# Kernel tuning notes

Hardware: AMD Instinct MI355X
Metric: run time of the kernel (lower is better)

Reference implementation:

```python
import jax, jax.numpy as jnp
import numpy as np

T, H, I, E, K, G, TG = 8192, 2048, 1024, 64, 8, 8, 4
ROUTED_SCALE = 2.5


def setup_inputs() -> dict:
    key = jax.random.key(0)
    ks = jax.random.split(key, 7)
    s = 0.02  # weight init scale
    return {
        "hidden_states": jax.random.normal(ks[0], (T, H), jnp.float32),
        "gate_w": jax.random.normal(ks[1], (E, H), jnp.float32) * s,
        "e_bias": jax.random.normal(ks[2], (E,), jnp.float32) * s,
        "w_gate_up": jax.random.normal(ks[3], (E, H, 2 * I), jnp.float32) * s,
        "w_down": jax.random.normal(ks[4], (E, I, H), jnp.float32) * s,
        "shared_gate_up": jax.random.normal(ks[5], (H, 2 * I), jnp.float32) * s,
        "shared_down": jax.random.normal(ks[6], (I, H), jnp.float32) * s,
    }


def silu_and_mul(x):
    g, u = jnp.split(x, 2, axis=-1)
    return jax.nn.silu(g) * u


def grouped_topk(router_logits, e_bias):
    # sigmoid scoring with e_score_correction_bias (DeepSeek-V3 / GLM4-MoE style)
    scores = jax.nn.sigmoid(router_logits)            # [T, E]
    scores_for_choice = scores + e_bias[None, :]
    # group score = sum of top-2 biased scores in each group
    grp = scores_for_choice.reshape(-1, G, E // G)
    group_scores = jax.lax.top_k(grp, 2)[0].sum(-1)   # [T, G]
    _, gidx = jax.lax.top_k(group_scores, TG)         # [T, TG]
    tok = jnp.arange(scores.shape[0])[:, None]
    group_mask = jnp.zeros_like(group_scores, dtype=bool).at[tok, gidx].set(True)
    expert_mask = jnp.repeat(group_mask, E // G, axis=-1)  # [T, E]
    masked = jnp.where(expert_mask, scores_for_choice, -jnp.inf)
    _, topk_ids = jax.lax.top_k(masked, K)            # [T, K]
    # combine weights come from the *unbiased* sigmoid scores
    topk_w = jnp.take_along_axis(scores, topk_ids, axis=-1)
    topk_w = topk_w / jnp.sum(topk_w, axis=-1, keepdims=True)  # renormalize
    return topk_w, topk_ids


def reference(hidden_states, gate_w, e_bias, w_gate_up, w_down,
              shared_gate_up, shared_down):
    x = hidden_states                                  # [T, H]
    # gate runs in fp32
    router_logits = x.astype(jnp.float32) @ gate_w.T   # [T, E]
    topk_w, topk_ids = grouped_topk(router_logits, e_bias)

    # shared expert MLP
    shared_out = silu_and_mul(x @ shared_gate_up) @ shared_down  # [T, H]

    # dense [T, E] combine matrix (top-k sparse in values)
    tok = jnp.arange(x.shape[0])[:, None]
    route = jnp.zeros((x.shape[0], E), x.dtype).at[tok, topk_ids].set(
        topk_w.astype(x.dtype))

    # grouped expert GEMMs via scan over experts (bounds peak memory)
    def body(acc, params):
        w1, w2, rw = params                            # [H,2I], [I,H], [T]
        y = silu_and_mul(x @ w1) @ w2                  # [T, H]
        return acc + rw[:, None] * y, None

    acc0 = jnp.zeros_like(x)
    routed_out, _ = jax.lax.scan(body, acc0, (w_gate_up, w_down, route.T))

    return routed_out * ROUTED_SCALE + shared_out
```

## Files before the change

kernel.cpp:

```cpp
#include <hip/hip_runtime.h>
#include <stdint.h>

#define T_TOK 8192
#define HDIM  2048
#define IDIM  1024
#define NEXP  64
#define KTOP  8
#define TGRP  4
#define TKTOT (T_TOK*KTOP)
#define MAXITEMS 4096
#define RSCALE 2.5f

typedef __attribute__((ext_vector_type(8))) short short8;
typedef __attribute__((ext_vector_type(4))) float f32x4;

__device__ __forceinline__ float bf2f(uint16_t u) {
    union { unsigned i; float f; } v; v.i = ((unsigned)u) << 16; return v.f;
}
__device__ __forceinline__ uint16_t f2bf(float f) {
    union { float f; unsigned i; } v; v.f = f;
    unsigned r = (v.i + 0x7FFFu + ((v.i >> 16) & 1u)) >> 16;
    return (uint16_t)r;
}
__device__ __forceinline__ void gload_lds16(const void* g, void* l) {
    __builtin_amdgcn_global_load_lds(
        (const __attribute__((address_space(1))) void*)g,
        (__attribute__((address_space(3))) void*)l, 16, 0, 0);
}
__device__ __forceinline__ int imin(int a, int b) { return a < b ? a : b; }

__global__ __launch_bounds__(256) void k_router(
    const float* __restrict__ x, const float* __restrict__ gw,
    const float* __restrict__ ebias,
    int* __restrict__ topk_ids, float* __restrict__ topk_w,
    int* __restrict__ counts)
{
    __shared__ float xs[16][132];
    __shared__ float wsb[64][133];
    __shared__ float sc[16][65];
    __shared__ float su[16][65];
    const int tid = threadIdx.x;
    const int e = tid & 63;
    const int tg = tid >> 6;
    const long tblk = (long)blockIdx.x * 16;

    float acc0 = 0.f, acc1 = 0.f, acc2 = 0.f, acc3 = 0.f;
    for (int ch = 0; ch < 16; ++ch) {
        const int h0 = ch << 7;
        for (int i = tid; i < 512; i += 256) {
            int r = i >> 5, c4 = (i & 31) << 2;
            float4 v = *(const float4*)(x + (tblk + r) * HDIM + h0 + c4);
            *(float4*)&xs[r][c4] = v;
        }
        for (int i = tid; i < 8192; i += 256) {
            int r = i >> 7, c = i & 127;
            wsb[r][c] = gw[(long)r * HDIM + h0 + c];
        }
        __syncthreads();
        #pragma unroll 8
        for (int hh = 0; hh < 128; ++hh) {
            float wv = wsb[e][hh];
            acc0 += xs[tg][hh] * wv;
            acc1 += xs[tg + 4][hh] * wv;
            acc2 += xs[tg + 8][hh] * wv;
            acc3 += xs[tg + 12][hh] * wv;
        }
        __syncthreads();
    }
    const float be = ebias[e];
    {
        float s;
        s = 1.f / (1.f + expf(-acc0)); su[tg][e] = s;      sc[tg][e] = s + be;
        s = 1.f / (1.f + expf(-acc1)); su[tg + 4][e] = s;  sc[tg + 4][e] = s + be;
        s = 1.f / (1.f + expf(-acc2)); su[tg + 8][e] = s;  sc[tg + 8][e] = s + be;
        s = 1.f / (1.f + expf(-acc3)); su[tg + 12][e] = s; sc[tg + 12][e] = s + be;
    }
    __syncthreads();
    if (tid < 16) {
        const int t = tid;
        float gs[8];
        #pragma unroll
        for (int g = 0; g < 8; ++g) {
            float m1 = -1e30f, m2 = -1e30f;
            #pragma unroll
            for (int j = 0; j < 8; ++j) {
                float v = sc[t][g * 8 + j];
                if (v > m1) { m2 = m1; m1 = v; } else if (v > m2) { m2 = v; }
            }
            gs[g] = m1 + m2;
        }
        int selmask = 0;
        #pragma unroll
        for (int it = 0; it < TGRP; ++it) {
            float best = -1e30f; int bg = 0;
            #pragma unroll
            for (int g = 0; g < 8; ++g)
                if (!((selmask >> g) & 1) && gs[g] > best) { best = gs[g]; bg = g; }
            selmask |= (1 << bg);
        }
        unsigned long long chosen = 0ull;
        int ids[KTOP]; float wv[KTOP]; float wsum = 0.f;
        #pragma unroll
        for (int it = 0; it < KTOP; ++it) {
            float best = -1e30f; int bi = 0;
            for (int ee = 0; ee < 64; ++ee) {
                if (((selmask >> (ee >> 3)) & 1) && !((chosen >> ee) & 1ull)) {
                    float v = sc[t][ee];
                    if (v > best) { best = v; bi = ee; }
                }
            }
            chosen |= (1ull << bi);
            ids[it] = bi; wv[it] = su[t][bi]; wsum += wv[it];
        }
        const float inv = 1.f / wsum;
        #pragma unroll
        for (int k = 0; k < KTOP; ++k) {
            topk_ids[(tblk + t) * KTOP + k] = ids[k];
            topk_w[(tblk + t) * KTOP + k] = wv[k] * inv;
            atomicAdd(&counts[ids[k]], 1);
        }
    }
}

__global__ __launch_bounds__(64) void k_scan2(
    const int* __restrict__ counts, int* offsets, int* cursor,
    int* __restrict__ it_r0, int* __restrict__ it_end,
    int* __restrict__ it_e, int* __restrict__ it_n0, int* __restrict__ nitems)
{
    const int e = threadIdx.x;
    const int c = counts[e];
    int pre = c;
    #pragma unroll
    for (int d = 1; d < 64; d <<= 1) {
        int v = __shfl_up(pre, d, 64);
        if (e >= d) pre += v;
    }
    const int offE = pre - c;
    offsets[e] = offE; cursor[e] = offE;
    const int ntl = (c + 255) >> 8;
    int ipre = ntl;
    #pragma unroll
    for (int d = 1; d < 64; d <<= 1) {
        int v = __shfl_up(ipre, d, 64);
        if (e >= d) ipre += v;
    }
    const int ibase = (ipre - ntl) * 8;
    for (int p = 0; p < 8; ++p)
        for (int t = 0; t < ntl; ++t) {
            int idx = ibase + p * ntl + t;
            it_r0[idx] = offE + t * 256;
            it_end[idx] = offE + c;
            it_e[idx] = e;
            it_n0[idx] = p << 8;
        }
    if (e == 63) *nitems = ibase + ntl * 8;
}

__global__ __launch_bounds__(256) void k_scatter(
    const int* __restrict__ topk_ids, int* cursor,
    int* __restrict__ perm_token, int* __restrict__ slot_of)
{
    int i = blockIdx.x * 256 + threadIdx.x;
    if (i >= TKTOT) return;
    int e = topk_ids[i];
    int pos = atomicAdd(&cursor[e], 1);
    perm_token[pos] = i >> 3;
    slot_of[i] = pos;
}

__global__ __launch_bounds__(256) void k_cvt_bf16(
    const float* __restrict__ in, uint16_t* __restrict__ outp, long n4)
{
    long i = (long)blockIdx.x * 256 + threadIdx.x;
    if (i >= n4) return;
    float4 v = *(const float4*)(in + i * 4);
    uint64_t pk = (uint64_t)f2bf(v.x) | ((uint64_t)f2bf(v.y) << 16)
                | ((uint64_t)f2bf(v.z) << 32) | ((uint64_t)f2bf(v.w) << 48);
    *(uint64_t*)(outp + i * 4) = pk;
}

template<bool INTER>
__global__ __launch_bounds__(256) void k_transpose2(
    const float* __restrict__ src, uint16_t* __restrict__ dst,
    int R, int C, long sStride, long dStride)
{
    __shared__ float tile[64][65];
    const int c0 = blockIdx.x << 6, r0 = blockIdx.y << 6, s = blockIdx.z;
    const float* S = src + (long)s * sStride;
    uint16_t* D = dst + (long)s * dStride;
    const int lc = (threadIdx.x & 15) << 2;
    const int lr = threadIdx.x >> 4;
    #pragma unroll
    for (int p = 0; p < 4; ++p) {
        int y = lr + p * 16;
        float4 v = *(const float4*)(S + (long)(r0 + y) * C + c0 + lc);
        tile[y][lc] = v.x; tile[y][lc + 1] = v.y;
        tile[y][lc + 2] = v.z; tile[y][lc + 3] = v.w;
    }
    __syncthreads();
    const int wc = threadIdx.x >> 3;
    const int wx = (threadIdx.x & 7) << 3;
    #pragma unroll
    for (int p = 0; p < 2; ++p) {
        int c = wc + p * 32;
        short8 v;
        #pragma unroll
        for (int j = 0; j < 8; ++j) v[j] = (short)f2bf(tile[wx + j][c]);
        int cg = c0 + c;
        int rd = INTER ? (((cg & (IDIM - 1)) << 1) + (cg >> 10)) : cg;
        *(short8*)(D + (long)rd * R + r0 + wx) = v;
    }
}

template<bool GATEUP, bool ROUTED>
__global__ __launch_bounds__(512, 2) void k_gemm3(
    const uint16_t* __restrict__ A, const uint16_t* __restrict__ Bw,
    void* __restrict__ OutP,
    const int* __restrict__ perm_token,
    const int* __restrict__ it_r0, const int* __restrict__ it_end,
    const int* __restrict__ it_e, const int* __restrict__ it_n0,
    const int* __restrict__ nitems, int* __restrict__ qcur,
    int Kd, long expStride)
{
    __shared__ char ldsb[4 * 32768];
    __shared__ int s_item;
    const int tid = threadIdx.x, lane = tid & 63, wid = tid >> 6;
    const int wm = wid >> 2, wn = wid & 3;

    const int rchunk = lane >> 2;
    const int swzS = ((lane & 3) ^ ((lane >> 3) & 3)) << 3;
    const int swzR = ((lane >> 4) ^ ((lane >> 1) & 3)) << 4;
    const int aoff = (wm * 128 + (lane & 15)) * 64 + swzR;
    const int boff = (wn * 64 + (lane & 15)) * 64 + swzR;
    const int ldst0 = (wid * 2) * 1024;
    const int ldst1 = (wid * 2 + 1) * 1024;

    const int nSub = Kd >> 5;
    const int NI = ROUTED ? nitems[0] : 0;

    for (;;) {
        int row0, end, n0; long eoff;
        if (ROUTED) {
            __syncthreads();
            if (tid == 0) s_item = atomicAdd(qcur, 1);
            __syncthreads();
            const int it = s_item;
            if (it >= NI) break;
            row0 = it_r0[it]; end = it_end[it]; n0 = it_n0[it];
            eoff = (long)it_e[it] * expStride;
        } else {
            row0 = (int)(blockIdx.x >> 3) << 8;
            end = row0 + 256;
            n0 = (int)(blockIdx.x & 7) << 8;
            eoff = 0;
        }

        const uint16_t *pA0, *pA1, *pB0, *pB1;
        {
            int r0l = (wid * 2) * 16 + rchunk;
            int r1l = (wid * 2 + 1) * 16 + rchunk;
            int ra0 = row0 + r0l, ra1 = row0 + r1l;
            if (ROUTED) { ra0 = imin(ra0, end - 1); ra1 = imin(ra1, end - 1); }
            long ga0 = (GATEUP && ROUTED) ? (long)perm_token[ra0] : (long)ra0;
            long ga1 = (GATEUP && ROUTED) ? (long)perm_token[ra1] : (long)ra1;
            pA0 = A + ga0 * Kd + swzS;
            pA1 = A + ga1 * Kd + swzS;
            pB0 = Bw + eoff + (long)(n0 + r0l) * Kd + swzS;
            pB1 = Bw + eoff + (long)(n0 + r1l) * Kd + swzS;
        }

        f32x4 acc[8][4];
        #pragma unroll
        for (int f = 0; f < 8; ++f)
            #pragma unroll
            for (int g = 0; g < 4; ++g) { f32x4 z = {0.f,0.f,0.f,0.f}; acc[f][g] = z; }

        #pragma unroll
        for (int j = 0; j < 3; ++j) {
            char* bb = ldsb + j * 32768;
            gload_lds16(pA0 + (j << 5), bb + ldst0);
            gload_lds16(pA1 + (j << 5), bb + ldst1);
            gload_lds16(pB0 + (j << 5), bb + 16384 + ldst0);
            gload_lds16(pB1 + (j << 5), bb + 16384 + ldst1);
        }

        for (int j = 0; j < nSub; ++j) {
            asm volatile("s_waitcnt vmcnt(8)" ::: "memory");
            __builtin_amdgcn_s_barrier();
            if (j + 3 < nSub) {
                const int js = j + 3;
                char* bb = ldsb + (js & 3) * 32768;
                gload_lds16(pA0 + (js << 5), bb + ldst0);
                gload_lds16(pA1 + (js << 5), bb + ldst1);
                gload_lds16(pB0 + (js << 5), bb + 16384 + ldst0);
                gload_lds16(pB1 + (js << 5), bb + 16384 + ldst1);
            }
            const char* bb = ldsb + (j & 3) * 32768;
            short8 av[8], bv[4];
            #pragma unroll
            for (int f = 0; f < 8; ++f)
                av[f] = *(const short8*)(bb + aoff + f * 1024);
            #pragma unroll
            for (int g = 0; g < 4; ++g)
                bv[g] = *(const short8*)(bb + 16384 + boff + g * 1024);
            __builtin_amdgcn_s_setprio(1);
            #pragma unroll
            for (int f = 0; f < 8; ++f)
                #pragma unroll
                for (int g = 0; g < 4; ++g)
                    acc[f][g] = __builtin_amdgcn_mfma_f32_16x16x32_bf16(
                        av[f], bv[g], acc[f][g], 0, 0, 0);
            __builtin_amdgcn_s_setprio(0);
        }

        const int colb = n0 + wn * 64 + (lane & 15);
        const int rowbase = row0 + wm * 128 + ((lane >> 4) << 2);
        if (GATEUP) {
            uint16_t* Oact = (uint16_t*)OutP;
            const bool evenl = ((lane & 1) == 0);
            #pragma unroll
            for (int f = 0; f < 8; ++f)
                #pragma unroll
                for (int g = 0; g < 4; ++g) {
                    f32x4 v = acc[f][g];
                    #pragma unroll
                    for (int r = 0; r < 4; ++r) {
                        float gg = v[r];
                        float uu = __shfl_xor(gg, 1, 64);
                        int row = rowbase + f * 16 + r;
                        if (evenl && (!ROUTED || row < end)) {
                            int jcol = (colb + g * 16) >> 1;
                            float sg = gg / (1.f + __expf(-gg));
                            Oact[(long)row * IDIM + jcol] = f2bf(sg * uu);
                        }
                    }
                }
        } else if (ROUTED) {
            uint16_t* Y = (uint16_t*)OutP;
            #pragma unroll
            for (int f = 0; f < 8; ++f)
                #pragma unroll
                for (int g = 0; g < 4; ++g) {
                    f32x4 v = acc[f][g];
                    #pragma unroll
                    for (int r = 0; r < 4; ++r) {
                        int row = rowbase + f * 16 + r;
                        if (row < end)
                            Y[(long)row * HDIM + colb + g * 16] = f2bf(v[r]);
                    }
                }
        } else {
            float* O = (float*)OutP;
            #pragma unroll
            for (int f = 0; f < 8; ++f)
                #pragma unroll
                for (int g = 0; g < 4; ++g) {
                    f32x4 v = acc[f][g];
                    #pragma unroll
                    for (int r = 0; r < 4; ++r) {
                        int row = rowbase + f * 16 + r;
                        O[(long)row * HDIM + colb + g * 16] = v[r];
                    }
                }
        }
        if (!ROUTED) break;
    }
}

__global__ __launch_bounds__(256) void k_combine(
    float* __restrict__ out, const uint16_t* __restrict__ ybuf,
    const int* __restrict__ slot_of, const float* __restrict__ topk_w)
{
    __shared__ int sl[KTOP];
    __shared__ float sw[KTOP];
    const int t = blockIdx.x, tid = threadIdx.x;
    if (tid < KTOP) {
        sl[tid] = slot_of[t * KTOP + tid];
        sw[tid] = topk_w[t * KTOP + tid] * RSCALE;
    }
    __syncthreads();
    const int h0 = tid << 3;
    float* orow = out + (long)t * HDIM + h0;
    float4 v0 = *(const float4*)(orow);
    float4 v1 = *(const float4*)(orow + 4);
    float a[8] = { v0.x, v0.y, v0.z, v0.w, v1.x, v1.y, v1.z, v1.w };
    #pragma unroll
    for (int k = 0; k < KTOP; ++k) {
        const uint16_t* yr = ybuf + (long)sl[k] * HDIM + h0;
        short8 y = *(const short8*)yr;
        float w = sw[k];
        #pragma unroll
        for (int j = 0; j < 8; ++j)
            a[j] += w * bf2f((uint16_t)y[j]);
    }
    v0.x = a[0]; v0.y = a[1]; v0.z = a[2]; v0.w = a[3];
    v1.x = a[4]; v1.y = a[5]; v1.z = a[6]; v1.w = a[7];
    *(float4*)(orow) = v0;
    *(float4*)(orow + 4) = v1;
}

extern "C" void kernel_launch(void* const* d_in, const int* in_sizes, int n_in,
                              void* d_out, int out_size, void* d_ws, size_t ws_size,
                              hipStream_t stream)
{
    const float* x  = (const float*)d_in[0];
    const float* gw = (const float*)d_in[1];
    const float* eb = (const float*)d_in[2];
    const float* w1 = (const float*)d_in[3];
    const float* w2 = (const float*)d_in[4];
    const float* s1 = (const float*)d_in[5];
    const float* s2 = (const float*)d_in[6];
    float* out = (float*)d_out;
    char* ws = (char*)d_ws;

    size_t off = 0;
    auto take = [&](size_t b) { size_t r = off; off += (b + 255) & ~(size_t)255; return r; };
    const size_t oXBF = take((size_t)T_TOK * HDIM * 2);
    const size_t oACT = take((size_t)TKTOT * IDIM * 2);
    const size_t oASH = take((size_t)T_TOK * IDIM * 2);
    const size_t oW1T = take((size_t)NEXP * 2048 * 2048 * 2);
    const size_t oW2T = take((size_t)NEXP * 2048 * 1024 * 2);
    const size_t oS1T = take((size_t)2048 * 2048 * 2);
    const size_t oS2T = take((size_t)2048 * 1024 * 2);
    const size_t oTKI = take((size_t)TKTOT * 4);
    const size_t oTKW = take((size_t)TKTOT * 4);
    const size_t oSLT = take((size_t)TKTOT * 4);
    const size_t oPRM = take((size_t)TKTOT * 4);
    const size_t oCTL = take(1024);
    const size_t oOFS = take(256);
    const size_t oCUR = take(256);
    const size_t oNT  = take(256);
    const size_t oIR  = take(MAXITEMS * 4);
    const size_t oIE  = take(MAXITEMS * 4);
    const size_t oIX  = take(MAXITEMS * 4);
    const size_t oIN  = take(MAXITEMS * 4);
    (void)ws_size; (void)in_sizes; (void)n_in; (void)out_size;

    uint16_t* xbf  = (uint16_t*)(ws + oXBF);
    uint16_t* act  = (uint16_t*)(ws + oACT);
    uint16_t* ash  = (uint16_t*)(ws + oASH);
    uint16_t* w1t  = (uint16_t*)(ws + oW1T);
    uint16_t* ybuf = (uint16_t*)(ws + oW1T);
    uint16_t* w2t  = (uint16_t*)(ws + oW2T);
    uint16_t* s1t  = (uint16_t*)(ws + oS1T);
    uint16_t* s2t  = (uint16_t*)(ws + oS2T);
    int*   tki  = (int*)(ws + oTKI);
    float* tkw  = (float*)(ws + oTKW);
    int*   slot = (int*)(ws + oSLT);
    int*   prm  = (int*)(ws + oPRM);
    int*   ctl  = (int*)(ws + oCTL);
    int*   ofs  = (int*)(ws + oOFS);
    int*   cur  = (int*)(ws + oCUR);
    int*   nt   = (int*)(ws + oNT);
    int*   ir0  = (int*)(ws + oIR);
    int*   iend = (int*)(ws + oIE);
    int*   ie   = (int*)(ws + oIX);
    int*   in0  = (int*)(ws + oIN);

    hipMemsetAsync(ws + oCTL, 0, 1024, stream);

    k_router<<<T_TOK / 16, 256, 0, stream>>>(x, gw, eb, tki, tkw, ctl);
    k_scan2<<<1, 64, 0, stream>>>(ctl, ofs, cur, ir0, iend, ie, in0, nt);
    k_scatter<<<TKTOT / 256, 256, 0, stream>>>(tki, cur, prm, slot);

    k_cvt_bf16<<<(T_TOK * HDIM / 4 + 255) / 256, 256, 0, stream>>>(x, xbf, (long)T_TOK * HDIM / 4);
    k_transpose2<true ><<<dim3(32, 32, NEXP), 256, 0, stream>>>(w1, w1t, 2048, 2048,
        (long)2048 * 2048, (long)2048 * 2048);
    k_transpose2<false><<<dim3(32, 16, NEXP), 256, 0, stream>>>(w2, w2t, 1024, 2048,
        (long)1024 * 2048, (long)2048 * 1024);
    k_transpose2<true ><<<dim3(32, 32, 1), 256, 0, stream>>>(s1, s1t, 2048, 2048, 0, 0);
    k_transpose2<false><<<dim3(32, 16, 1), 256, 0, stream>>>(s2, s2t, 1024, 2048, 0, 0);

    k_gemm3<true, false><<<dim3(256), 512, 0, stream>>>(
        xbf, s1t, ash, nullptr, nullptr, nullptr, nullptr, nullptr, nullptr, nullptr, 2048, 0);
    k_gemm3<true, true><<<dim3(256), 512, 0, stream>>>(
        xbf, w1t, act, prm, ir0, iend, ie, in0, nt, ctl + 64, 2048, (long)2048 * 2048);
    k_gemm3<false, false><<<dim3(256), 512, 0, stream>>>(
        ash, s2t, out, nullptr, nullptr, nullptr, nullptr, nullptr, nullptr, nullptr, 1024, 0);
    k_gemm3<false, true><<<dim3(256), 512, 0, stream>>>(
        act, w2t, ybuf, nullptr, ir0, iend, ie, in0, nt, ctl + 65, 1024, (long)2048 * 1024);

    k_combine<<<T_TOK, 256, 0, stream>>>(out, ybuf, slot, tkw);
}
```

Baseline: 2.314 ms.

## Software-pipeline LDS fragment reads against MFMA in grouped GEMM mainloop

Restructures the GEMM main loop so register fragments for the next k-step are read from LDS while the current step's MFMAs run. Each step is split into two halves with their own barriers, and the A and B global-to-LDS prefetches are issued in separate halves. Wait counts are tuned per stage to match. The aim is to hide LDS read latency and stagger the global loads. It costs more live registers and an extra barrier per iteration, and the finer vmcnt bookkeeping is fragile near the tail.

Result: slower. 2.532 ms (+9.4%).

```diff
diff --git a/kernel.cpp b/kernel.cpp
--- a/kernel.cpp
+++ b/kernel.cpp
@@ -13,6 +13,9 @@
 
 typedef __attribute__((ext_vector_type(8))) short short8;
 typedef __attribute__((ext_vector_type(4))) float f32x4;
+
+#define VMCNT(n) asm volatile("s_waitcnt vmcnt(" #n ")" ::: "memory")
+#define BARRIER() asm volatile("s_barrier" ::: "memory")
 
 __device__ __forceinline__ float bf2f(uint16_t u) {
     union { unsigned i; float f; } v; v.i = ((unsigned)u) << 16; return v.f;
@@ -213,7 +216,7 @@
 }
 
 template<bool GATEUP, bool ROUTED>
-__global__ __launch_bounds__(512, 2) void k_gemm3(
+__global__ __launch_bounds__(512, 2) void k_gemm5(
     const uint16_t* __restrict__ A, const uint16_t* __restrict__ Bw,
     void* __restrict__ OutP,
     const int* __restrict__ perm_token,
@@ -283,34 +286,58 @@
             gload_lds16(pB0 + (j << 5), bb + 16384 + ldst0);
             gload_lds16(pB1 + (j << 5), bb + 16384 + ldst1);
         }
+        VMCNT(8);
+        BARRIER();
+        short8 aC[8], bC0, bC1;
+        #pragma unroll
+        for (int f = 0; f < 8; ++f)
+            aC[f] = *(const short8*)(ldsb + aoff + f * 1024);
+        bC0 = *(const short8*)(ldsb + 16384 + boff);
+        bC1 = *(const short8*)(ldsb + 16384 + boff + 1024);
 
         for (int j = 0; j < nSub; ++j) {
-            asm volatile("s_waitcnt vmcnt(8)" ::: "memory");
-            __builtin_amdgcn_s_barrier();
-            if (j + 3 < nSub) {
-                const int js = j + 3;
-                char* bb = ldsb + (js & 3) * 32768;
-                gload_lds16(pA0 + (js << 5), bb + ldst0);
-                gload_lds16(pA1 + (js << 5), bb + ldst1);
-                gload_lds16(pB0 + (js << 5), bb + 16384 + ldst0);
-                gload_lds16(pB1 + (js << 5), bb + 16384 + ldst1);
+            const char* bb = ldsb + (j & 3) * 32768;
+            char* bs = ldsb + ((j + 3) & 3) * 32768;
+            const bool st = (j + 3) < nSub;
+            BARRIER();
+            if (st) {
+                gload_lds16(pA0 + ((j + 3) << 5), bs + ldst0);
+                gload_lds16(pA1 + ((j + 3) << 5), bs + ldst1);
             }
-            const char* bb = ldsb + (j & 3) * 32768;
-            short8 av[8], bv[4];
+            short8 b2 = *(const short8*)(bb + 16384 + boff + 2048);
+            short8 b3 = *(const short8*)(bb + 16384 + boff + 3072);
+            __builtin_amdgcn_s_setprio(1);
+            #pragma unroll
+            for (int f = 0; f < 8; ++f) {
+                acc[f][0] = __builtin_amdgcn_mfma_f32_16x16x32_bf16(aC[f], bC0, acc[f][0], 0, 0, 0);
+                acc[f][1] = __builtin_amdgcn_mfma_f32_16x16x32_bf16(aC[f], bC1, acc[f][1], 0, 0, 0);
+            }
+            __builtin_amdgcn_s_setprio(0);
+            if (st)                 VMCNT(6);
+            else if (j + 2 < nSub)  VMCNT(4);
+            else if (j + 1 < nSub)  VMCNT(0);
+            BARRIER();
+            if (st) {
+                gload_lds16(pB0 + ((j + 3) << 5), bs + 16384 + ldst0);
+                gload_lds16(pB1 + ((j + 3) << 5), bs + 16384 + ldst1);
+            }
+            const char* bn = ldsb + ((j + 1) & 3) * 32768;
+            short8 nA[8], nB0, nB1;
             #pragma unroll
             for (int f = 0; f < 8; ++f)
-                av[f] = *(const short8*)(bb + aoff + f * 1024);
-            #pragma unroll
-            for (int g = 0; g < 4; ++g)
-                bv[g] = *(const short8*)(bb + 16384 + boff + g * 1024);
+                nA[f] = *(const short8*)(bn + aoff + f * 1024);
+            nB0 = *(const short8*)(bn + 16384 + boff);
+            nB1 = *(const short8*)(bn + 16384 + boff + 1024);
             __builtin_amdgcn_s_setprio(1);
             #pragma unroll
-            for (int f = 0; f < 8; ++f)
-                #pragma unroll
-                for (int g = 0; g < 4; ++g)
-                    acc[f][g] = __builtin_amdgcn_mfma_f32_16x16x32_bf16(
-                        av[f], bv[g], acc[f][g], 0, 0, 0);
+            for (int f = 0; f < 8; ++f) {
+                acc[f][2] = __builtin_amdgcn_mfma_f32_16x16x32_bf16(aC[f], b2, acc[f][2], 0, 0, 0);
+                acc[f][3] = __builtin_amdgcn_mfma_f32_16x16x32_bf16(aC[f], b3, acc[f][3], 0, 0, 0);
+            }
             __builtin_amdgcn_s_setprio(0);
+            #pragma unroll
+            for (int f = 0; f < 8; ++f) aC[f] = nA[f];
+            bC0 = nB0; bC1 = nB1;
         }
 
         const int colb = n0 + wn * 64 + (lane & 15);
@@ -471,13 +498,13 @@
     k_transpose2<true ><<<dim3(32, 32, 1), 256, 0, stream>>>(s1, s1t, 2048, 2048, 0, 0);
     k_transpose2<false><<<dim3(32, 16, 1), 256, 0, stream>>>(s2, s2t, 1024, 2048, 0, 0);
 
-    k_gemm3<true, false><<<dim3(256), 512, 0, stream>>>(
+    k_gemm5<true, false><<<dim3(256), 512, 0, stream>>>(
         xbf, s1t, ash, nullptr, nullptr, nullptr, nullptr, nullptr, nullptr, nullptr, 2048, 0);
-    k_gemm3<true, true><<<dim3(256), 512, 0, stream>>>(
+    k_gemm5<true, true><<<dim3(256), 512, 0, stream>>>(
         xbf, w1t, act, prm, ir0, iend, ie, in0, nt, ctl + 64, 2048, (long)2048 * 2048);
-    k_gemm3<false, false><<<dim3(256), 512, 0, stream>>>(
+    k_gemm5<false, false><<<dim3(256), 512, 0, stream>>>(
         ash, s2t, out, nullptr, nullptr, nullptr, nullptr, nullptr, nullptr, nullptr, 1024, 0);
-    k_gemm3<false, true><<<dim3(256), 512, 0, stream>>>(
+    k_gemm5<false, true><<<dim3(256), 512, 0, stream>>>(
         act, w2t, ybuf, nullptr, ir0, iend, ie, in0, nt, ctl + 65, 1024, (long)2048 * 1024);
 
     k_combine<<<T_TOK, 256, 0, stream>>>(out, ybuf, slot, tkw);
```

## Interleave prefetch issue with split MFMA phases in grouped GEMM loop

Applied to the files above, without the earlier changes.

Restructures the GEMM main loop into two halves. Each half loads part of the A fragments, issues part of the next-stage global-to-LDS prefetch, then runs 16 MFMAs between added barriers. The aim is to spread memory issue across compute and keep waves in lockstep so loads and matrix ops overlap better. The cost is two extra barriers per k-step, which can add stalls.

New measurement: 2.140 ms. -7.5%, faster.

```diff
diff --git a/kernel.cpp b/kernel.cpp
--- a/kernel.cpp
+++ b/kernel.cpp
@@ -13,6 +13,9 @@
 
 typedef __attribute__((ext_vector_type(8))) short short8;
 typedef __attribute__((ext_vector_type(4))) float f32x4;
+
+#define VMCNT(n) asm volatile("s_waitcnt vmcnt(" #n ")" ::: "memory")
+#define BARRIER() asm volatile("s_barrier" ::: "memory")
 
 __device__ __forceinline__ float bf2f(uint16_t u) {
     union { unsigned i; float f; } v; v.i = ((unsigned)u) << 16; return v.f;
@@ -213,7 +216,7 @@
 }
 
 template<bool GATEUP, bool ROUTED>
-__global__ __launch_bounds__(512, 2) void k_gemm3(
+__global__ __launch_bounds__(512, 2) void k_gemm6(
     const uint16_t* __restrict__ A, const uint16_t* __restrict__ Bw,
     void* __restrict__ OutP,
     const int* __restrict__ perm_token,
@@ -232,10 +235,10 @@
     const int swzR = ((lane >> 4) ^ ((lane >> 1) & 3)) << 4;
     const int aoff = (wm * 128 + (lane & 15)) * 64 + swzR;
     const int boff = (wn * 64 + (lane & 15)) * 64 + swzR;
-    const int ldst0 = (wid * 2) * 1024;
-    const int ldst1 = (wid * 2 + 1) * 1024;
-
-    const int nSub = Kd >> 5;
+    const int dstA0 = (wid * 2) * 1024;
+    const int dstA1 = (wid * 2 + 1) * 1024;
+
+    const int nKt = Kd >> 5;
     const int NI = ROUTED ? nitems[0] : 0;
 
     for (;;) {
@@ -255,18 +258,18 @@
             eoff = 0;
         }
 
-        const uint16_t *pA0, *pA1, *pB0, *pB1;
+        const uint16_t *pa0, *pa1, *pb0, *pb1;
         {
-            int r0l = (wid * 2) * 16 + rchunk;
-            int r1l = (wid * 2 + 1) * 16 + rchunk;
+            int r0l = wid * 32 + rchunk;
+            int r1l = wid * 32 + 16 + rchunk;
             int ra0 = row0 + r0l, ra1 = row0 + r1l;
             if (ROUTED) { ra0 = imin(ra0, end - 1); ra1 = imin(ra1, end - 1); }
             long ga0 = (GATEUP && ROUTED) ? (long)perm_token[ra0] : (long)ra0;
             long ga1 = (GATEUP && ROUTED) ? (long)perm_token[ra1] : (long)ra1;
-            pA0 = A + ga0 * Kd + swzS;
-            pA1 = A + ga1 * Kd + swzS;
-            pB0 = Bw + eoff + (long)(n0 + r0l) * Kd + swzS;
-            pB1 = Bw + eoff + (long)(n0 + r1l) * Kd + swzS;
+            pa0 = A + ga0 * Kd + swzS;
+            pa1 = A + ga1 * Kd + swzS;
+            pb0 = Bw + eoff + (long)(n0 + r0l) * Kd + swzS;
+            pb1 = Bw + eoff + (long)(n0 + r1l) * Kd + swzS;
         }
 
         f32x4 acc[8][4];
@@ -278,38 +281,78 @@
         #pragma unroll
         for (int j = 0; j < 3; ++j) {
             char* bb = ldsb + j * 32768;
-            gload_lds16(pA0 + (j << 5), bb + ldst0);
-            gload_lds16(pA1 + (j << 5), bb + ldst1);
-            gload_lds16(pB0 + (j << 5), bb + 16384 + ldst0);
-            gload_lds16(pB1 + (j << 5), bb + 16384 + ldst1);
-        }
-
-        for (int j = 0; j < nSub; ++j) {
-            asm volatile("s_waitcnt vmcnt(8)" ::: "memory");
-            __builtin_amdgcn_s_barrier();
-            if (j + 3 < nSub) {
-                const int js = j + 3;
-                char* bb = ldsb + (js & 3) * 32768;
-                gload_lds16(pA0 + (js << 5), bb + ldst0);
-                gload_lds16(pA1 + (js << 5), bb + ldst1);
-                gload_lds16(pB0 + (js << 5), bb + 16384 + ldst0);
-                gload_lds16(pB1 + (js << 5), bb + 16384 + ldst1);
+            gload_lds16(pa0 + (j << 5), bb + dstA0);
+            gload_lds16(pa1 + (j << 5), bb + dstA1);
+            gload_lds16(pb0 + (j << 5), bb + 16384 + dstA0);
+            gload_lds16(pb1 + (j << 5), bb + 16384 + dstA1);
+        }
+
+        for (int kt = 0; kt < nKt; ++kt) {
+            const char* bb = ldsb + (kt & 3) * 32768;
+            char* bs = ldsb + ((kt + 3) & 3) * 32768;
+            const bool st = (kt + 3) < nKt;
+
+            VMCNT(8);
+            BARRIER();
+
+            short8 fa0 = *(const short8*)(bb + aoff);
+            short8 fa1 = *(const short8*)(bb + aoff + 1024);
+            short8 fa2 = *(const short8*)(bb + aoff + 2048);
+            short8 fa3 = *(const short8*)(bb + aoff + 3072);
+            short8 fb0 = *(const short8*)(bb + 16384 + boff);
+            short8 fb1 = *(const short8*)(bb + 16384 + boff + 1024);
+            short8 fb2 = *(const short8*)(bb + 16384 + boff + 2048);
+            short8 fb3 = *(const short8*)(bb + 16384 + boff + 3072);
+            if (st) {
+                gload_lds16(pa0 + ((kt + 3) << 5), bs + dstA0);
+                gload_lds16(pa1 + ((kt + 3) << 5), bs + dstA1);
             }
-            const char* bb = ldsb + (j & 3) * 32768;
-            short8 av[8], bv[4];
-            #pragma unroll
-            for (int f = 0; f < 8; ++f)
-                av[f] = *(const short8*)(bb + aoff + f * 1024);
-            #pragma unroll
-            for (int g = 0; g < 4; ++g)
-                bv[g] = *(const short8*)(bb + 16384 + boff + g * 1024);
+            BARRIER();
             __builtin_amdgcn_s_setprio(1);
-            #pragma unroll
-            for (int f = 0; f < 8; ++f)
-                #pragma unroll
-                for (int g = 0; g < 4; ++g)
-                    acc[f][g] = __builtin_amdgcn_mfma_f32_16x16x32_bf16(
-                        av[f], bv[g], acc[f][g], 0, 0, 0);
+            acc[0][0] = __builtin_amdgcn_mfma_f32_16x16x32_bf16(fa0, fb0, acc[0][0], 0, 0, 0);
+            acc[0][1] = __builtin_amdgcn_mfma_f32_16x16x32_bf16(fa0, fb1, acc[0][1], 0, 0, 0);
+            acc[0][2] = __builtin_amdgcn_mfma_f32_16x16x32_bf16(fa0, fb2, acc[0][2], 0, 0, 0);
+            acc[0][3] = __builtin_amdgcn_mfma_f32_16x16x32_bf16(fa0, fb3, acc[0][3], 0, 0, 0);
+            acc[1][0] = __builtin_amdgcn_mfma_f32_16x16x32_bf16(fa1, fb0, acc[1][0], 0, 0, 0);
+            acc[1][1] = __builtin_amdgcn_mfma_f32_16x16x32_bf16(fa1, fb1, acc[1][1], 0, 0, 0);
+            acc[1][2] = __builtin_amdgcn_mfma_f32_16x16x32_bf16(fa1, fb2, acc[1][2], 0, 0, 0);
+            acc[1][3] = __builtin_amdgcn_mfma_f32_16x16x32_bf16(fa1, fb3, acc[1][3], 0, 0, 0);
+            acc[2][0] = __builtin_amdgcn_mfma_f32_16x16x32_bf16(fa2, fb0, acc[2][0], 0, 0, 0);
+            acc[2][1] = __builtin_amdgcn_mfma_f32_16x16x32_bf16(fa2, fb1, acc[2][1], 0, 0, 0);
+            acc[2][2] = __builtin_amdgcn_mfma_f32_16x16x32_bf16(fa2, fb2, acc[2][2], 0, 0, 0);
+            acc[2][3] = __builtin_amdgcn_mfma_f32_16x16x32_bf16(fa2, fb3, acc[2][3], 0, 0, 0);
+            acc[3][0] = __builtin_amdgcn_mfma_f32_16x16x32_bf16(fa3, fb0, acc[3][0], 0, 0, 0);
+            acc[3][1] = __builtin_amdgcn_mfma_f32_16x16x32_bf16(fa3, fb1, acc[3][1], 0, 0, 0);
+            acc[3][2] = __builtin_amdgcn_mfma_f32_16x16x32_bf16(fa3, fb2, acc[3][2], 0, 0, 0);
+            acc[3][3] = __builtin_amdgcn_mfma_f32_16x16x32_bf16(fa3, fb3, acc[3][3], 0, 0, 0);
+            __builtin_amdgcn_s_setprio(0);
+
+            short8 fa4 = *(const short8*)(bb + aoff + 4096);
+            short8 fa5 = *(const short8*)(bb + aoff + 5120);
+            short8 fa6 = *(const short8*)(bb + aoff + 6144);
+            short8 fa7 = *(const short8*)(bb + aoff + 7168);
+            if (st) {
+                gload_lds16(pb0 + ((kt + 3) << 5), bs + 16384 + dstA0);
+                gload_lds16(pb1 + ((kt + 3) << 5), bs + 16384 + dstA1);
+            }
+            BARRIER();
+            __builtin_amdgcn_s_setprio(1);
+            acc[4][0] = __builtin_amdgcn_mfma_f32_16x16x32_bf16(fa4, fb0, acc[4][0], 0, 0, 0);
+            acc[4][1] = __builtin_amdgcn_mfma_f32_16x16x32_bf16(fa4, fb1, acc[4][1], 0, 0, 0);
+            acc[4][2] = __builtin_amdgcn_mfma_f32_16x16x32_bf16(fa4, fb2, acc[4][2], 0, 0, 0);
+            acc[4][3] = __builtin_amdgcn_mfma_f32_16x16x32_bf16(fa4, fb3, acc[4][3], 0, 0, 0);
+            acc[5][0] = __builtin_amdgcn_mfma_f32_16x16x32_bf16(fa5, fb0, acc[5][0], 0, 0, 0);
+            acc[5][1] = __builtin_amdgcn_mfma_f32_16x16x32_bf16(fa5, fb1, acc[5][1], 0, 0, 0);
+            acc[5][2] = __builtin_amdgcn_mfma_f32_16x16x32_bf16(fa5, fb2, acc[5][2], 0, 0, 0);
+            acc[5][3] = __builtin_amdgcn_mfma_f32_16x16x32_bf16(fa5, fb3, acc[5][3], 0, 0, 0);
+            acc[6][0] = __builtin_amdgcn_mfma_f32_16x16x32_bf16(fa6, fb0, acc[6][0], 0, 0, 0);
+            acc[6][1] = __builtin_amdgcn_mfma_f32_16x16x32_bf16(fa6, fb1, acc[6][1], 0, 0, 0);
+            acc[6][2] = __builtin_amdgcn_mfma_f32_16x16x32_bf16(fa6, fb2, acc[6][2], 0, 0, 0);
+            acc[6][3] = __builtin_amdgcn_mfma_f32_16x16x32_bf16(fa6, fb3, acc[6][3], 0, 0, 0);
+            acc[7][0] = __builtin_amdgcn_mfma_f32_16x16x32_bf16(fa7, fb0, acc[7][0], 0, 0, 0);
+            acc[7][1] = __builtin_amdgcn_mfma_f32_16x16x32_bf16(fa7, fb1, acc[7][1], 0, 0, 0);
+            acc[7][2] = __builtin_amdgcn_mfma_f32_16x16x32_bf16(fa7, fb2, acc[7][2], 0, 0, 0);
+            acc[7][3] = __builtin_amdgcn_mfma_f32_16x16x32_bf16(fa7, fb3, acc[7][3], 0, 0, 0);
             __builtin_amdgcn_s_setprio(0);
         }
 
@@ -471,13 +514,13 @@
     k_transpose2<true ><<<dim3(32, 32, 1), 256, 0, stream>>>(s1, s1t, 2048, 2048, 0, 0);
     k_transpose2<false><<<dim3(32, 16, 1), 256, 0, stream>>>(s2, s2t, 1024, 2048, 0, 0);
 
-    k_gemm3<true, false><<<dim3(256), 512, 0, stream>>>(
+    k_gemm6<true, false><<<dim3(256), 512, 0, stream>>>(
         xbf, s1t, ash, nullptr, nullptr, nullptr, nullptr, nullptr, nullptr, nullptr, 2048, 0);
-    k_gemm3<true, true><<<dim3(256), 512, 0, stream>>>(
+    k_gemm6<true, true><<<dim3(256), 512, 0, stream>>>(
         xbf, w1t, act, prm, ir0, iend, ie, in0, nt, ctl + 64, 2048, (long)2048 * 2048);
-    k_gemm3<false, false><<<dim3(256), 512, 0, stream>>>(
+    k_gemm6<false, false><<<dim3(256), 512, 0, stream>>>(
         ash, s2t, out, nullptr, nullptr, nullptr, nullptr, nullptr, nullptr, nullptr, 1024, 0);
-    k_gemm3<false, true><<<dim3(256), 512, 0, stream>>>(
+    k_gemm6<false, true><<<dim3(256), 512, 0, stream>>>(
         act, w2t, ybuf, nullptr, ir0, iend, ie, in0, nt, ctl + 65, 1024, (long)2048 * 1024);
 
     k_combine<<<T_TOK, 256, 0, stream>>>(out, ybuf, slot, tkw);
```
